# Performance work log

Hardware: AMD Instinct MI355X
Metric: run time of the kernel (lower is better)

Reference implementation:

```python
import jax, jax.numpy as jnp
import numpy as np

B, TOPK, H, I, E = 128, 8, 2048, 1408, 16


def setup_inputs() -> dict:
    key = jax.random.key(0)
    ks = jax.random.split(key, 8)
    x = jax.random.normal(ks[0], (B, H), dtype=jnp.float32)
    expert_ids = jax.random.randint(ks[1], (B, TOPK), 0, E, dtype=jnp.int32)
    smooth_scales = jax.random.uniform(ks[2], (E, I), dtype=jnp.float32, minval=0.5, maxval=1.5)
    expert_scales = jax.random.uniform(ks[3], (B, TOPK), dtype=jnp.float32)
    expert_scales = expert_scales / jnp.sum(expert_scales, axis=-1, keepdims=True)
    x_active_mask = jnp.ones((B,), dtype=bool)
    # int8-valued quantized expert weights (stored int32 for portability)
    w1 = jax.random.randint(ks[4], (E, H, 2 * I), -127, 128, dtype=jnp.int32)
    w1_scale = jax.random.uniform(ks[5], (E, 2 * I), dtype=jnp.float32, minval=1e-3, maxval=1e-2)
    w2 = jax.random.randint(ks[6], (E, I, H), -127, 128, dtype=jnp.int32)
    w2_scale = jax.random.uniform(ks[7], (E, H), dtype=jnp.float32, minval=1e-3, maxval=1e-2)
    return {"x": x, "expert_ids": expert_ids, "smooth_scales": smooth_scales,
            "expert_scales": expert_scales, "x_active_mask": x_active_mask,
            "w1": w1, "w1_scale": w1_scale, "w2": w2, "w2_scale": w2_scale}


def reference(x, expert_ids, smooth_scales, expert_scales, x_active_mask,
              w1, w1_scale, w2, w2_scale):
    # --- dispatch: dynamic per-token int8 quantization of x ---
    sx = jnp.maximum(jnp.max(jnp.abs(x), axis=-1, keepdims=True), 1e-12) / 127.0  # [B,1]
    xq = jnp.round(jnp.clip(x / sx, -128.0, 127.0))  # int8 values, fp32 storage
    # --- grouped GEMM1 (dense-equivalent of per-expert grouped matmul) ---
    h = jnp.einsum('bh,ehf->bef', xq, w1.astype(jnp.float32))  # [B,E,2I] int32 accum
    h = h * sx[:, :, None] * w1_scale[None]  # dequant: x_scale * per-channel w_scale
    # --- SwiGLU activation ---
    gate, up = h[..., :I], h[..., I:]
    act = jax.nn.silu(gate) * up  # [B,E,I]
    # --- smooth + dynamic re-quantization for GEMM2 ---
    act = act * smooth_scales[None]  # [B,E,I]
    s2 = jnp.maximum(jnp.max(jnp.abs(act), axis=-1, keepdims=True), 1e-12) / 127.0  # [B,E,1]
    aq = jnp.round(jnp.clip(act / s2, -128.0, 127.0))
    # --- grouped GEMM2 + dequant ---
    o = jnp.einsum('bei,eih->beh', aq, w2.astype(jnp.float32))  # [B,E,H]
    o = o * s2 * w2_scale[None]
    # --- combine: weighted sum over routed experts (scatter expert_scales to one-hot) ---
    comb = jnp.zeros((x.shape[0], w1.shape[0]), dtype=x.dtype)
    comb = comb.at[jnp.arange(x.shape[0])[:, None], expert_ids].add(expert_scales)  # [B,E]
    y = jnp.einsum('beh,be->bh', o, comb)
    return y * x_active_mask[:, None].astype(y.dtype)
```

## Files before the change

### kernel.cpp

```cpp
#include <hip/hip_runtime.h>
#include <math.h>

#define NB 128
#define NTOPK 8
#define NH 2048
#define NI 1408
#define NE 16
#define NTWO_I 2816
#define RR 16
#define NCF 7
#define SLOTS_PER_E (NCF * RR)
#define MAXSLOTS (NE * SLOTS_PER_E)

#define LDS_REG 260

typedef int v4i __attribute__((ext_vector_type(4)));

__device__ __forceinline__ int pack4(int a, int b, int c, int d) {
    return (a & 0xff) | ((b & 0xff) << 8) | ((c & 0xff) << 16) | (d << 24);
}

__device__ __forceinline__ void gload_lds16(const int* g, int* l) {
    __builtin_amdgcn_global_load_lds(
        (const __attribute__((address_space(1))) void*)(const void*)g,
        (__attribute__((address_space(3))) void*)(void*)l, 16, 0, 0);
}

__global__ void k_quant_x(const float* __restrict__ x,
                          int* __restrict__ xq8d,
                          float* __restrict__ sxv) {
    int b = blockIdx.x;
    int t = threadIdx.x;
    const float* xr = x + (size_t)b * NH;
    float m = 0.0f;
    for (int j = t; j < NH; j += 256) m = fmaxf(m, fabsf(xr[j]));
    __shared__ float red[256];
    red[t] = m;
    __syncthreads();
    for (int s = 128; s > 0; s >>= 1) {
        if (t < s) red[t] = fmaxf(red[t], red[t + s]);
        __syncthreads();
    }
    float scale = fmaxf(red[0], 1e-12f) / 127.0f;
    if (t == 0) sxv[b] = scale;
    for (int g = t; g < NH / 4; g += 256) {
        int q[4];
#pragma unroll
        for (int u = 0; u < 4; ++u)
            q[u] = (int)rintf(fminf(fmaxf(xr[4 * g + u] / scale, -128.0f), 127.0f));
        xq8d[(size_t)b * (NH / 4) + g] = pack4(q[0], q[1], q[2], q[3]);
    }
}

__global__ void k_route(const int* __restrict__ expert_ids,
                        const float* __restrict__ expert_scales,
                        int* __restrict__ slot_b,
                        float* __restrict__ slot_w,
                        int* __restrict__ nce_arr) {
    __shared__ int cnt[NE];
    __shared__ int fill[NE];
    int t = threadIdx.x;
    if (t < NE) { cnt[t] = 0; fill[t] = 0; }
    __syncthreads();
    for (int p = t; p < NB * NTOPK; p += 256) atomicAdd(&cnt[expert_ids[p]], 1);
    __syncthreads();
    if (t < NE) {
        int c = (cnt[t] + RR - 1) / RR;
        nce_arr[t] = c < NCF ? c : NCF;
    }
    for (int s = t; s < MAXSLOTS; s += 256) {
        slot_b[s] = 0;
        slot_w[s] = 0.0f;
    }
    __syncthreads();
    for (int p = t; p < NB * NTOPK; p += 256) {
        int e = expert_ids[p];
        int pos = atomicAdd(&fill[e], 1);
        if (pos < SLOTS_PER_E) {
            slot_b[e * SLOTS_PER_E + pos] = p >> 3;
            slot_w[e * SLOTS_PER_E + pos] = expert_scales[p];
        }
    }
}

__global__ __launch_bounds__(256) void k_gemm1(
    const int* __restrict__ xq8d,
    const int* __restrict__ slot_b, const int* __restrict__ nce_arr,
    const int* __restrict__ w1, int* __restrict__ h) {
    __shared__ int smw[2][16 * LDS_REG];
    int e = blockIdx.y;
    int nce = nce_arr[e];
    if (nce == 0) return;
    int t = threadIdx.x;
    int wave = t >> 6;
    int lane = t & 63;
    int lm = lane & 15;
    int kl = lane >> 4;
    int slot0 = e * SLOTS_PER_E;
    int colb0 = blockIdx.x * 64;
    int colb = colb0 + wave * 16;

    int rb[NCF];
#pragma unroll
    for (int q = 0; q < NCF; ++q)
        rb[q] = (q < nce) ? slot_b[slot0 + q * RR + lm] : 0;

    const int* gq = w1 + (size_t)e * NH * NTWO_I
                    + (size_t)(wave * 16 + kl) * NTWO_I + colb0 + lm * 4;

    v4i acc[NCF];
#pragma unroll
    for (int q = 0; q < NCF; ++q) acc[q] = (v4i){0, 0, 0, 0};

#define PH1(BUF, KB, SCOND, SBUF, SKB)                                          \
    do {                                                                        \
        v4i av[NCF];                                                            \
        _Pragma("unroll")                                                       \
        for (int q = 0; q < NCF; ++q)                                           \
            if (q < nce)                                                        \
                av[q] = *(const v4i*)(xq8d + (size_t)rb[q] * (NH / 4)           \
                                      + (KB) * 16 + kl * 4);                    \
        if (SCOND) {                                                            \
            const int* gs = gq + (size_t)(SKB) * 64 * NTWO_I;                   \
            _Pragma("unroll")                                                   \
            for (int i = 0; i < 4; ++i)                                         \
                gload_lds16(gs + (size_t)(i * 4) * NTWO_I,                      \
                            &smw[SBUF][(wave * 4 + i) * LDS_REG]);              \
        }                                                                       \
        int wv[16];                                                             \
        _Pragma("unroll")                                                       \
        for (int j = 0; j < 16; ++j)                                            \
            wv[j] = smw[BUF][(kl * 4 + (j >> 2)) * LDS_REG + (j & 3) * 64       \
                             + wave * 16 + lm];                                 \
        v4i bf = {pack4(wv[0], wv[1], wv[2], wv[3]),                            \
                  pack4(wv[4], wv[5], wv[6], wv[7]),                            \
                  pack4(wv[8], wv[9], wv[10], wv[11]),                          \
                  pack4(wv[12], wv[13], wv[14], wv[15])};                       \
        _Pragma("unroll")                                                       \
        for (int q = 0; q < NCF; ++q)                                           \
            if (q < nce)                                                        \
                acc[q] = __builtin_amdgcn_mfma_i32_16x16x64_i8(av[q], bf,       \
                                                               acc[q], 0, 0, 0);\
        __syncthreads();                                                        \
    } while (0)

#pragma unroll
    for (int i = 0; i < 4; ++i)
        gload_lds16(gq + (size_t)(i * 4) * NTWO_I,
                    &smw[0][(wave * 4 + i) * LDS_REG]);
    __syncthreads();

    for (int kb = 0; kb < NH / 64; kb += 2) {
        PH1(0, kb, true, 1, kb + 1);
        PH1(1, kb + 1, (kb + 2 < NH / 64), 0, kb + 2);
    }
#undef PH1

#pragma unroll
    for (int q = 0; q < NCF; ++q) {
        if (q < nce) {
            int* hp = h + (size_t)(slot0 + q * RR) * NTWO_I + colb + lm;
#pragma unroll
            for (int r = 0; r < 4; ++r)
                hp[(size_t)(kl * 4 + r) * NTWO_I] = acc[q][r];
        }
    }
}

__global__ void k_act(const int* __restrict__ h, const float* __restrict__ sxv,
                      const int* __restrict__ slot_b, const int* __restrict__ nce_arr,
                      const float* __restrict__ w1_scale, const float* __restrict__ smooth,
                      int* __restrict__ aq8d, float* __restrict__ s2f) {
    int slot = blockIdx.x;
    int e = slot / SLOTS_PER_E;
    int within = slot - e * SLOTS_PER_E;
    if ((within >> 4) >= nce_arr[e]) return;
    int t = threadIdx.x;
    float sx = sxv[slot_b[slot]];
    const int* hr = h + (size_t)slot * NTWO_I;
    const float* w1s = w1_scale + (size_t)e * NTWO_I;
    const float* sm = smooth + (size_t)e * NI;

    float av[8];
    float m = 0.0f;
    int it = 0;
    for (int g = t; g < NI / 4; g += 256, ++it) {
        v4i gv = *(const v4i*)(hr + 4 * g);
        v4i uv = *(const v4i*)(hr + NI + 4 * g);
#pragma unroll
        for (int u = 0; u < 4; ++u) {
            int j = 4 * g + u;
            float gt = (float)gv[u] * sx * w1s[j];
            float up = (float)uv[u] * sx * w1s[j + NI];
            float a = (gt / (1.0f + expf(-gt))) * up * sm[j];
            av[it * 4 + u] = a;
            m = fmaxf(m, fabsf(a));
        }
    }
    __shared__ float red[256];
    red[t] = m;
    __syncthreads();
    for (int s = 128; s > 0; s >>= 1) {
        if (t < s) red[t] = fmaxf(red[t], red[t + s]);
        __syncthreads();
    }
    float s2 = fmaxf(red[0], 1e-12f) / 127.0f;
    if (t == 0) s2f[slot] = s2;
    it = 0;
    for (int g = t; g < NI / 4; g += 256, ++it) {
        int q[4];
#pragma unroll
        for (int u = 0; u < 4; ++u)
            q[u] = (int)rintf(fminf(fmaxf(av[it * 4 + u] / s2, -128.0f), 127.0f));
        aq8d[(size_t)slot * (NI / 4) + g] = pack4(q[0], q[1], q[2], q[3]);
    }
}

__global__ __launch_bounds__(256) void k_gemm2(
    const int* __restrict__ aq8d, const float* __restrict__ s2f,
    const int* __restrict__ slot_b, const float* __restrict__ slot_w,
    const int* __restrict__ nce_arr,
    const int* __restrict__ w2, const float* __restrict__ w2_scale,
    float* __restrict__ y) {
    __shared__ int smw[2][16 * LDS_REG];
    int e = blockIdx.y;
    int nce = nce_arr[e];
    if (nce == 0) return;
    int t = threadIdx.x;
    int wave = t >> 6;
    int lane = t & 63;
    int lm = lane & 15;
    int kl = lane >> 4;
    int slot0 = e * SLOTS_PER_E;
    int colb0 = blockIdx.x * 64;
    int colb = colb0 + wave * 16;

    const int* gq = w2 + (size_t)e * NI * NH
                    + (size_t)(wave * 16 + kl) * NH + colb0 + lm * 4;

    v4i acc[NCF];
#pragma unroll
    for (int q = 0; q < NCF; ++q) acc[q] = (v4i){0, 0, 0, 0};

#define PH2(BUF, KB, SCOND, SBUF, SKB)                                          \
    do {                                                                        \
        v4i av[NCF];                                                            \
        _Pragma("unroll")                                                       \
        for (int q = 0; q < NCF; ++q)                                           \
            if (q < nce)                                                        \
                av[q] = *(const v4i*)(aq8d                                      \
                         + (size_t)(slot0 + q * RR + lm) * (NI / 4)             \
                         + (KB) * 16 + kl * 4);                                 \
        if (SCOND) {                                                            \
            const int* gs = gq + (size_t)(SKB) * 64 * NH;                       \
            _Pragma("unroll")                                                   \
            for (int i = 0; i < 4; ++i)                                         \
                gload_lds16(gs + (size_t)(i * 4) * NH,                          \
                            &smw[SBUF][(wave * 4 + i) * LDS_REG]);              \
        }                                                                       \
        int wv[16];                                                             \
        _Pragma("unroll")                                                       \
        for (int j = 0; j < 16; ++j)                                            \
            wv[j] = smw[BUF][(kl * 4 + (j >> 2)) * LDS_REG + (j & 3) * 64       \
                             + wave * 16 + lm];                                 \
        v4i bf = {pack4(wv[0], wv[1], wv[2], wv[3]),                            \
                  pack4(wv[4], wv[5], wv[6], wv[7]),                            \
                  pack4(wv[8], wv[9], wv[10], wv[11]),                          \
                  pack4(wv[12], wv[13], wv[14], wv[15])};                       \
        _Pragma("unroll")                                                       \
        for (int q = 0; q < NCF; ++q)                                           \
            if (q < nce)                                                        \
                acc[q] = __builtin_amdgcn_mfma_i32_16x16x64_i8(av[q], bf,       \
                                                               acc[q], 0, 0, 0);\
        __syncthreads();                                                        \
    } while (0)

#pragma unroll
    for (int i = 0; i < 4; ++i)
        gload_lds16(gq + (size_t)(i * 4) * NH,
                    &smw[0][(wave * 4 + i) * LDS_REG]);
    __syncthreads();

    for (int kb = 0; kb < NI / 64; kb += 2) {
        PH2(0, kb, true, 1, kb + 1);
        PH2(1, kb + 1, (kb + 2 < NI / 64), 0, kb + 2);
    }
#undef PH2

    float w2s = w2_scale[(size_t)e * NH + colb + lm];
#pragma unroll
    for (int q = 0; q < NCF; ++q) {
        if (q < nce) {
#pragma unroll
            for (int r = 0; r < 4; ++r) {
                int s = slot0 + q * RR + kl * 4 + r;
                float cf = s2f[s] * slot_w[s];
                if (cf != 0.0f)
                    atomicAdd(y + (size_t)slot_b[s] * NH + colb + lm,
                              (float)acc[q][r] * cf * w2s);
            }
        }
    }
}

extern "C" void kernel_launch(void* const* d_in, const int* in_sizes, int n_in,
                              void* d_out, int out_size, void* d_ws, size_t ws_size,
                              hipStream_t stream) {
    const float* x = (const float*)d_in[0];
    const int* expert_ids = (const int*)d_in[1];
    const float* smooth = (const float*)d_in[2];
    const float* expert_scales = (const float*)d_in[3];
    const int* w1 = (const int*)d_in[5];
    const float* w1_scale = (const float*)d_in[6];
    const int* w2 = (const int*)d_in[7];
    const float* w2_scale = (const float*)d_in[8];
    float* y = (float*)d_out;

    char* p = (char*)d_ws;
    int* xq8d = (int*)p;               p += (size_t)NB * (NH / 4) * 4;
    float* sxv = (float*)p;            p += NB * 4;
    int* slot_b = (int*)p;             p += MAXSLOTS * 4;
    float* slot_w = (float*)p;         p += MAXSLOTS * 4;
    int* nce_arr = (int*)p;            p += NE * 4;
    float* s2f = (float*)p;            p += MAXSLOTS * 4;
    int* h = (int*)p;                  p += (size_t)MAXSLOTS * NTWO_I * 4;
    int* aq8d = (int*)p;               p += (size_t)MAXSLOTS * (NI / 4) * 4;

    hipMemsetAsync(d_out, 0, (size_t)out_size * sizeof(float), stream);

    k_quant_x<<<NB, 256, 0, stream>>>(x, xq8d, sxv);
    k_route<<<1, 256, 0, stream>>>(expert_ids, expert_scales, slot_b, slot_w, nce_arr);
    dim3 g1(NTWO_I / 64, NE);
    k_gemm1<<<g1, 256, 0, stream>>>(xq8d, slot_b, nce_arr, w1, h);
    k_act<<<MAXSLOTS, 256, 0, stream>>>(h, sxv, slot_b, nce_arr, w1_scale, smooth,
                                        aq8d, s2f);
    dim3 g2(NH / 64, NE);
    k_gemm2<<<g2, 256, 0, stream>>>(aq8d, s2f, slot_b, slot_w, nce_arr,
                                    w2, w2_scale, y);
}
```

Baseline: 665.3 us.

## Prefetch activation fragments one step ahead and use partial vmcnt waits

Both grouped GEMM kernels now load the activation A-fragments for the next k-block into a second register set while the current block's MFMAs run. The full __syncthreads is replaced by explicit s_waitcnt vmcnt(11) plus s_barrier, so only the previous stage's loads must land before use. This hides global-load latency for A and lets the weight LDS loads overlap compute. It also loads all NCF fragments whatever nce is, and depends on the hand-counted vmcnt being exactly right. The x-quantization kernel is vectorized to float4 loads held in registers and uses a reciprocal multiply instead of a division.

```diff
diff --git a/kernel.cpp b/kernel.cpp
--- a/kernel.cpp
+++ b/kernel.cpp
@@ -15,6 +15,7 @@
 #define LDS_REG 260
 
 typedef int v4i __attribute__((ext_vector_type(4)));
+typedef float v4f __attribute__((ext_vector_type(4)));
 
 __device__ __forceinline__ int pack4(int a, int b, int c, int d) {
     return (a & 0xff) | ((b & 0xff) << 8) | ((c & 0xff) << 16) | (d << 24);
@@ -33,7 +34,13 @@
     int t = threadIdx.x;
     const float* xr = x + (size_t)b * NH;
     float m = 0.0f;
-    for (int j = t; j < NH; j += 256) m = fmaxf(m, fabsf(xr[j]));
+    v4f xv[2];
+#pragma unroll
+    for (int it = 0; it < 2; ++it) {
+        xv[it] = *(const v4f*)(xr + 4 * (t + 256 * it));
+#pragma unroll
+        for (int u = 0; u < 4; ++u) m = fmaxf(m, fabsf(xv[it][u]));
+    }
     __shared__ float red[256];
     red[t] = m;
     __syncthreads();
@@ -43,12 +50,14 @@
     }
     float scale = fmaxf(red[0], 1e-12f) / 127.0f;
     if (t == 0) sxv[b] = scale;
-    for (int g = t; g < NH / 4; g += 256) {
+    float inv = 1.0f / scale;
+#pragma unroll
+    for (int it = 0; it < 2; ++it) {
         int q[4];
 #pragma unroll
         for (int u = 0; u < 4; ++u)
-            q[u] = (int)rintf(fminf(fmaxf(xr[4 * g + u] / scale, -128.0f), 127.0f));
-        xq8d[(size_t)b * (NH / 4) + g] = pack4(q[0], q[1], q[2], q[3]);
+            q[u] = (int)rintf(fminf(fmaxf(xv[it][u] * inv, -128.0f), 127.0f));
+        xq8d[(size_t)b * (NH / 4) + t + 256 * it] = pack4(q[0], q[1], q[2], q[3]);
     }
 }
 
@@ -112,26 +121,30 @@
 #pragma unroll
     for (int q = 0; q < NCF; ++q) acc[q] = (v4i){0, 0, 0, 0};
 
-#define PH1(BUF, KB, SCOND, SBUF, SKB)                                          \
+    v4i avA[NCF], avB[NCF];
+
+#define PH1(CBUF, PC, NBUF, NKB, AVC, AVN)                                      \
     do {                                                                        \
-        v4i av[NCF];                                                            \
-        _Pragma("unroll")                                                       \
-        for (int q = 0; q < NCF; ++q)                                           \
-            if (q < nce)                                                        \
-                av[q] = *(const v4i*)(xq8d + (size_t)rb[q] * (NH / 4)           \
-                                      + (KB) * 16 + kl * 4);                    \
-        if (SCOND) {                                                            \
-            const int* gs = gq + (size_t)(SKB) * 64 * NTWO_I;                   \
+        if (PC) {                                                               \
+            _Pragma("unroll")                                                   \
+            for (int q = 0; q < NCF; ++q)                                       \
+                AVN[q] = *(const v4i*)(xq8d + (size_t)rb[q] * (NH / 4)          \
+                                       + (NKB) * 16 + kl * 4);                  \
+            const int* gs = gq + (size_t)(NKB) * 64 * NTWO_I;                   \
             _Pragma("unroll")                                                   \
             for (int i = 0; i < 4; ++i)                                         \
                 gload_lds16(gs + (size_t)(i * 4) * NTWO_I,                      \
-                            &smw[SBUF][(wave * 4 + i) * LDS_REG]);              \
+                            &smw[NBUF][(wave * 4 + i) * LDS_REG]);              \
+            asm volatile("s_waitcnt vmcnt(11)" ::: "memory");                   \
+        } else {                                                                \
+            asm volatile("s_waitcnt vmcnt(0)" ::: "memory");                    \
         }                                                                       \
+        __builtin_amdgcn_s_barrier();                                           \
         int wv[16];                                                             \
         _Pragma("unroll")                                                       \
         for (int j = 0; j < 16; ++j)                                            \
-            wv[j] = smw[BUF][(kl * 4 + (j >> 2)) * LDS_REG + (j & 3) * 64       \
-                             + wave * 16 + lm];                                 \
+            wv[j] = smw[CBUF][(kl * 4 + (j >> 2)) * LDS_REG + (j & 3) * 64      \
+                              + wave * 16 + lm];                                \
         v4i bf = {pack4(wv[0], wv[1], wv[2], wv[3]),                            \
                   pack4(wv[4], wv[5], wv[6], wv[7]),                            \
                   pack4(wv[8], wv[9], wv[10], wv[11]),                          \
@@ -139,20 +152,23 @@
         _Pragma("unroll")                                                       \
         for (int q = 0; q < NCF; ++q)                                           \
             if (q < nce)                                                        \
-                acc[q] = __builtin_amdgcn_mfma_i32_16x16x64_i8(av[q], bf,       \
+                acc[q] = __builtin_amdgcn_mfma_i32_16x16x64_i8(AVC[q], bf,      \
                                                                acc[q], 0, 0, 0);\
-        __syncthreads();                                                        \
+        asm volatile("s_waitcnt lgkmcnt(0)" ::: "memory");                      \
+        __builtin_amdgcn_s_barrier();                                           \
     } while (0)
 
+#pragma unroll
+    for (int q = 0; q < NCF; ++q)
+        avA[q] = *(const v4i*)(xq8d + (size_t)rb[q] * (NH / 4) + kl * 4);
 #pragma unroll
     for (int i = 0; i < 4; ++i)
         gload_lds16(gq + (size_t)(i * 4) * NTWO_I,
                     &smw[0][(wave * 4 + i) * LDS_REG]);
-    __syncthreads();
 
     for (int kb = 0; kb < NH / 64; kb += 2) {
-        PH1(0, kb, true, 1, kb + 1);
-        PH1(1, kb + 1, (kb + 2 < NH / 64), 0, kb + 2);
+        PH1(0, true, 1, kb + 1, avA, avB);
+        PH1(1, (kb + 2 < NH / 64), 0, kb + 2, avB, avA);
     }
 #undef PH1
 
@@ -237,32 +253,38 @@
 
     const int* gq = w2 + (size_t)e * NI * NH
                     + (size_t)(wave * 16 + kl) * NH + colb0 + lm * 4;
+    const int* ab[NCF];
+#pragma unroll
+    for (int q = 0; q < NCF; ++q)
+        ab[q] = aq8d + (size_t)(slot0 + q * RR + lm) * (NI / 4) + kl * 4;
 
     v4i acc[NCF];
 #pragma unroll
     for (int q = 0; q < NCF; ++q) acc[q] = (v4i){0, 0, 0, 0};
 
-#define PH2(BUF, KB, SCOND, SBUF, SKB)                                          \
+    v4i avA[NCF], avB[NCF];
+
+#define PH2(CBUF, PC, NBUF, NKB, AVC, AVN)                                      \
     do {                                                                        \
-        v4i av[NCF];                                                            \
-        _Pragma("unroll")                                                       \
-        for (int q = 0; q < NCF; ++q)                                           \
-            if (q < nce)                                                        \
-                av[q] = *(const v4i*)(aq8d                                      \
-                         + (size_t)(slot0 + q * RR + lm) * (NI / 4)             \
-                         + (KB) * 16 + kl * 4);                                 \
-        if (SCOND) {                                                            \
-            const int* gs = gq + (size_t)(SKB) * 64 * NH;                       \
+        if (PC) {                                                               \
+            _Pragma("unroll")                                                   \
+            for (int q = 0; q < NCF; ++q)                                       \
+                AVN[q] = *(const v4i*)(ab[q] + (NKB) * 16);                     \
+            const int* gs = gq + (size_t)(NKB) * 64 * NH;                       \
             _Pragma("unroll")                                                   \
             for (int i = 0; i < 4; ++i)                                         \
                 gload_lds16(gs + (size_t)(i * 4) * NH,                          \
-                            &smw[SBUF][(wave * 4 + i) * LDS_REG]);              \
+                            &smw[NBUF][(wave * 4 + i) * LDS_REG]);              \
+            asm volatile("s_waitcnt vmcnt(11)" ::: "memory");                   \
+        } else {                                                                \
+            asm volatile("s_waitcnt vmcnt(0)" ::: "memory");                    \
         }                                                                       \
+        __builtin_amdgcn_s_barrier();                                           \
         int wv[16];                                                             \
         _Pragma("unroll")                                                       \
         for (int j = 0; j < 16; ++j)                                            \
-            wv[j] = smw[BUF][(kl * 4 + (j >> 2)) * LDS_REG + (j & 3) * 64       \
-                             + wave * 16 + lm];                                 \
+            wv[j] = smw[CBUF][(kl * 4 + (j >> 2)) * LDS_REG + (j & 3) * 64      \
+                              + wave * 16 + lm];                                \
         v4i bf = {pack4(wv[0], wv[1], wv[2], wv[3]),                            \
                   pack4(wv[4], wv[5], wv[6], wv[7]),                            \
                   pack4(wv[8], wv[9], wv[10], wv[11]),                          \
@@ -270,20 +292,22 @@
         _Pragma("unroll")                                                       \
         for (int q = 0; q < NCF; ++q)                                           \
             if (q < nce)                                                        \
-                acc[q] = __builtin_amdgcn_mfma_i32_16x16x64_i8(av[q], bf,       \
+                acc[q] = __builtin_amdgcn_mfma_i32_16x16x64_i8(AVC[q], bf,      \
                                                                acc[q], 0, 0, 0);\
-        __syncthreads();                                                        \
+        asm volatile("s_waitcnt lgkmcnt(0)" ::: "memory");                      \
+        __builtin_amdgcn_s_barrier();                                           \
     } while (0)
 
+#pragma unroll
+    for (int q = 0; q < NCF; ++q) avA[q] = *(const v4i*)(ab[q]);
 #pragma unroll
     for (int i = 0; i < 4; ++i)
         gload_lds16(gq + (size_t)(i * 4) * NH,
                     &smw[0][(wave * 4 + i) * LDS_REG]);
-    __syncthreads();
 
     for (int kb = 0; kb < NI / 64; kb += 2) {
-        PH2(0, kb, true, 1, kb + 1);
-        PH2(1, kb + 1, (kb + 2 < NI / 64), 0, kb + 2);
+        PH2(0, true, 1, kb + 1, avA, avB);
+        PH2(1, (kb + 2 < NI / 64), 0, kb + 2, avB, avA);
     }
 #undef PH2
 
```

Measured after the change: 681.1 us. 2.4% more time.

## Replace atomic scatter in GEMM2 with per-slot output buffer and gather combine kernel

Applied to the files above, without the earlier changes.

GEMM2 now writes scaled per-slot outputs to a workspace buffer instead of doing float atomicAdds into y. A new combine kernel gathers each token's up to eight slot rows through an inverse slot map built in routing. This also drops the output memset. Quant and activation kernels switch to vector loads, fully unrolled loops and reciprocal multiplies instead of divides. The trade is an extra kernel launch and an extra write and read of about 7 MB of slot outputs, in exchange for no atomic contention. Reciprocal multiplication can round differently from division at quantization boundaries.

```diff
diff --git a/kernel.cpp b/kernel.cpp
--- a/kernel.cpp
+++ b/kernel.cpp
@@ -15,6 +15,7 @@
 #define LDS_REG 260
 
 typedef int v4i __attribute__((ext_vector_type(4)));
+typedef float v4f __attribute__((ext_vector_type(4)));
 
 __device__ __forceinline__ int pack4(int a, int b, int c, int d) {
     return (a & 0xff) | ((b & 0xff) << 8) | ((c & 0xff) << 16) | (d << 24);
@@ -33,7 +34,13 @@
     int t = threadIdx.x;
     const float* xr = x + (size_t)b * NH;
     float m = 0.0f;
-    for (int j = t; j < NH; j += 256) m = fmaxf(m, fabsf(xr[j]));
+    v4f xv[2];
+#pragma unroll
+    for (int it = 0; it < 2; ++it) {
+        xv[it] = *(const v4f*)(xr + 4 * (t + 256 * it));
+#pragma unroll
+        for (int u = 0; u < 4; ++u) m = fmaxf(m, fabsf(xv[it][u]));
+    }
     __shared__ float red[256];
     red[t] = m;
     __syncthreads();
@@ -43,12 +50,14 @@
     }
     float scale = fmaxf(red[0], 1e-12f) / 127.0f;
     if (t == 0) sxv[b] = scale;
-    for (int g = t; g < NH / 4; g += 256) {
+    float inv = 1.0f / scale;
+#pragma unroll
+    for (int it = 0; it < 2; ++it) {
         int q[4];
 #pragma unroll
         for (int u = 0; u < 4; ++u)
-            q[u] = (int)rintf(fminf(fmaxf(xr[4 * g + u] / scale, -128.0f), 127.0f));
-        xq8d[(size_t)b * (NH / 4) + g] = pack4(q[0], q[1], q[2], q[3]);
+            q[u] = (int)rintf(fminf(fmaxf(xv[it][u] * inv, -128.0f), 127.0f));
+        xq8d[(size_t)b * (NH / 4) + t + 256 * it] = pack4(q[0], q[1], q[2], q[3]);
     }
 }
 
@@ -56,7 +65,8 @@
                         const float* __restrict__ expert_scales,
                         int* __restrict__ slot_b,
                         float* __restrict__ slot_w,
-                        int* __restrict__ nce_arr) {
+                        int* __restrict__ nce_arr,
+                        int* __restrict__ inv_slot) {
     __shared__ int cnt[NE];
     __shared__ int fill[NE];
     int t = threadIdx.x;
@@ -79,6 +89,9 @@
         if (pos < SLOTS_PER_E) {
             slot_b[e * SLOTS_PER_E + pos] = p >> 3;
             slot_w[e * SLOTS_PER_E + pos] = expert_scales[p];
+            inv_slot[p] = e * SLOTS_PER_E + pos;
+        } else {
+            inv_slot[p] = -1;
         }
     }
 }
@@ -181,10 +194,24 @@
     const float* w1s = w1_scale + (size_t)e * NTWO_I;
     const float* sm = smooth + (size_t)e * NI;
 
-    float av[8];
+    float a0[4], a1[4];
     float m = 0.0f;
-    int it = 0;
-    for (int g = t; g < NI / 4; g += 256, ++it) {
+    {
+        v4i gv = *(const v4i*)(hr + 4 * t);
+        v4i uv = *(const v4i*)(hr + NI + 4 * t);
+#pragma unroll
+        for (int u = 0; u < 4; ++u) {
+            int j = 4 * t + u;
+            float gt = (float)gv[u] * sx * w1s[j];
+            float up = (float)uv[u] * sx * w1s[j + NI];
+            float a = (gt / (1.0f + expf(-gt))) * up * sm[j];
+            a0[u] = a;
+            m = fmaxf(m, fabsf(a));
+        }
+    }
+    bool hasB = t < (NI / 4 - 256);
+    if (hasB) {
+        int g = t + 256;
         v4i gv = *(const v4i*)(hr + 4 * g);
         v4i uv = *(const v4i*)(hr + NI + 4 * g);
 #pragma unroll
@@ -193,7 +220,7 @@
             float gt = (float)gv[u] * sx * w1s[j];
             float up = (float)uv[u] * sx * w1s[j + NI];
             float a = (gt / (1.0f + expf(-gt))) * up * sm[j];
-            av[it * 4 + u] = a;
+            a1[u] = a;
             m = fmaxf(m, fabsf(a));
         }
     }
@@ -206,13 +233,20 @@
     }
     float s2 = fmaxf(red[0], 1e-12f) / 127.0f;
     if (t == 0) s2f[slot] = s2;
-    it = 0;
-    for (int g = t; g < NI / 4; g += 256, ++it) {
+    float inv = 1.0f / s2;
+    {
         int q[4];
 #pragma unroll
         for (int u = 0; u < 4; ++u)
-            q[u] = (int)rintf(fminf(fmaxf(av[it * 4 + u] / s2, -128.0f), 127.0f));
-        aq8d[(size_t)slot * (NI / 4) + g] = pack4(q[0], q[1], q[2], q[3]);
+            q[u] = (int)rintf(fminf(fmaxf(a0[u] * inv, -128.0f), 127.0f));
+        aq8d[(size_t)slot * (NI / 4) + t] = pack4(q[0], q[1], q[2], q[3]);
+    }
+    if (hasB) {
+        int q[4];
+#pragma unroll
+        for (int u = 0; u < 4; ++u)
+            q[u] = (int)rintf(fminf(fmaxf(a1[u] * inv, -128.0f), 127.0f));
+        aq8d[(size_t)slot * (NI / 4) + t + 256] = pack4(q[0], q[1], q[2], q[3]);
     }
 }
 
@@ -221,7 +255,7 @@
     const int* __restrict__ slot_b, const float* __restrict__ slot_w,
     const int* __restrict__ nce_arr,
     const int* __restrict__ w2, const float* __restrict__ w2_scale,
-    float* __restrict__ y) {
+    float* __restrict__ o) {
     __shared__ int smw[2][16 * LDS_REG];
     int e = blockIdx.y;
     int nce = nce_arr[e];
@@ -294,12 +328,33 @@
 #pragma unroll
             for (int r = 0; r < 4; ++r) {
                 int s = slot0 + q * RR + kl * 4 + r;
-                float cf = s2f[s] * slot_w[s];
-                if (cf != 0.0f)
-                    atomicAdd(y + (size_t)slot_b[s] * NH + colb + lm,
-                              (float)acc[q][r] * cf * w2s);
+                o[(size_t)s * NH + colb + lm] =
+                    (float)acc[q][r] * (s2f[s] * slot_w[s]) * w2s;
             }
         }
+    }
+}
+
+__global__ __launch_bounds__(256) void k_combine(
+    const float* __restrict__ o, const int* __restrict__ inv_slot,
+    float* __restrict__ y) {
+    int b = blockIdx.x;
+    int t = threadIdx.x;
+    int sl[NTOPK];
+#pragma unroll
+    for (int k = 0; k < NTOPK; ++k) sl[k] = inv_slot[b * NTOPK + k];
+#pragma unroll
+    for (int it = 0; it < NH / (256 * 4); ++it) {
+        int c = (t + 256 * it) * 4;
+        v4f accv = {0.0f, 0.0f, 0.0f, 0.0f};
+#pragma unroll
+        for (int k = 0; k < NTOPK; ++k) {
+            if (sl[k] >= 0) {
+                v4f ov = *(const v4f*)(o + (size_t)sl[k] * NH + c);
+                accv += ov;
+            }
+        }
+        *(v4f*)(y + (size_t)b * NH + c) = accv;
     }
 }
 
@@ -323,18 +378,20 @@
     float* slot_w = (float*)p;         p += MAXSLOTS * 4;
     int* nce_arr = (int*)p;            p += NE * 4;
     float* s2f = (float*)p;            p += MAXSLOTS * 4;
+    int* inv_slot = (int*)p;           p += (size_t)NB * NTOPK * 4;
     int* h = (int*)p;                  p += (size_t)MAXSLOTS * NTWO_I * 4;
     int* aq8d = (int*)p;               p += (size_t)MAXSLOTS * (NI / 4) * 4;
-
-    hipMemsetAsync(d_out, 0, (size_t)out_size * sizeof(float), stream);
+    float* o = (float*)p;              p += (size_t)MAXSLOTS * NH * 4;
 
     k_quant_x<<<NB, 256, 0, stream>>>(x, xq8d, sxv);
-    k_route<<<1, 256, 0, stream>>>(expert_ids, expert_scales, slot_b, slot_w, nce_arr);
+    k_route<<<1, 256, 0, stream>>>(expert_ids, expert_scales, slot_b, slot_w,
+                                   nce_arr, inv_slot);
     dim3 g1(NTWO_I / 64, NE);
     k_gemm1<<<g1, 256, 0, stream>>>(xq8d, slot_b, nce_arr, w1, h);
     k_act<<<MAXSLOTS, 256, 0, stream>>>(h, sxv, slot_b, nce_arr, w1_scale, smooth,
                                         aq8d, s2f);
     dim3 g2(NH / 64, NE);
     k_gemm2<<<g2, 256, 0, stream>>>(aq8d, s2f, slot_b, slot_w, nce_arr,
-                                    w2, w2_scale, y);
-}
+                                    w2, w2_scale, o);
+    k_combine<<<NB, 256, 0, stream>>>(o, inv_slot, y);
+}
```

New measurement: 655.0 us. No clear change (-1.5%).
